# Optimization experiments

Measured on AMD Instinct MI355X. Metric: run time of the kernel, lower is better.

Reference implementation:

```python
import jax, jax.numpy as jnp
import numpy as np

B, L, D, T = 32, 2048, 64, 512          # batch, seq_len, input_dim, pred steps
H, EK = 2, 64                           # num_heads, embed_dim_per_head
E = H * EK                              # embed_dim = 128
P = 2                                   # function 'L' -> 2 coefficients
LAT, HID = 64, 64                       # latent_dim, hidden_dim
DIM = 2 * D                             # value dim after cat(X, M)


def setup_inputs() -> dict:
    key = jax.random.key(0)
    ks = jax.random.split(key, 20)
    s = 0.05
    inp = {
        "timesteps": jnp.sort(jax.random.uniform(ks[0], (B, L)), axis=-1),
        "X": jax.random.normal(ks[1], (B, L, D)),
        "M": jax.random.bernoulli(ks[2], 0.5, (B, L, D)).astype(jnp.float32),
        "y_time_steps": jnp.sort(jax.random.uniform(ks[3], (B, T)), axis=-1),
        # time_embedding: Linear(1, E)
        "te_w": jax.random.normal(ks[4], (1, E)) * s,
        "te_b": jax.random.normal(ks[5], (E,)) * s,
        # learned queries (1, P, E)
        "query": jax.random.normal(ks[6], (1, P, E)),
        # query_map / key_map: Linear(E, E), stored (in, out)
        "qm_w": jax.random.normal(ks[7], (E, E)) * s,
        "qm_b": jax.random.normal(ks[8], (E,)) * s,
        "km_w": jax.random.normal(ks[9], (E, E)) * s,
        "km_b": jax.random.normal(ks[10], (E,)) * s,
        # shared attention output head: Linear(2*D*H, LAT)
        "out_w": jax.random.normal(ks[11], (DIM * H, LAT)) * s,
        "out_b": jax.random.normal(ks[12], (LAT,)) * s,
        # decoder (depth=1): Linear(LAT, HID) -> ReLU -> Linear(HID, D)
        "dec_w1": jax.random.normal(ks[13], (LAT, HID)) * s,
        "dec_b1": jax.random.normal(ks[14], (HID,)) * s,
        "dec_w2": jax.random.normal(ks[15], (HID, D)) * s,
        "dec_b2": jax.random.normal(ks[16], (D,)) * s,
    }
    return inp


def _forward(timesteps, X, M, y_time_steps, te_w, te_b, query,
             qm_w, qm_b, km_w, km_b, out_w, out_b,
             dec_w1, dec_b1, dec_w2, dec_b2):
    # learn_time_embedding: Linear(1,E) then sin() on indices i % H == 0
    te = timesteps[..., None] @ te_w + te_b                 # (B, L, E)
    sin_idx = (jnp.arange(E) % H) == 0
    key_emb = jnp.where(sin_idx, jnp.sin(te), te)           # (B, L, E)

    value = jnp.concatenate([X, M], axis=-1)                # (B, L, 2D)
    mask = jnp.concatenate([M, M], axis=-1)                 # (B, L, 2D)

    q = query @ qm_w + qm_b                                 # (1, P, E)
    k = key_emb @ km_w + km_b                               # (B, L, E)
    qh = q.reshape(1, P, H, EK).transpose(0, 2, 1, 3)       # (1, H, P, EK)
    kh = k.reshape(B, L, H, EK).transpose(0, 2, 1, 3)       # (B, H, L, EK)

    scores = jnp.einsum('xhpe,bhle->bhpl', qh, kh) / jnp.sqrt(jnp.float32(EK))
    # score broadcast over value dim + per-feature mask fill (-1e9 as in torch)
    logits = jnp.where(mask[:, None, None, :, :] == 0, -1e9,
                       scores[..., None])                   # (B, H, P, L, 2D)
    p_attn = jax.nn.softmax(logits, axis=-2)                # softmax over L
    x = jnp.einsum('bhpld,bld->bhpd', p_attn, value)        # (B, H, P, 2D)

    x = x.transpose(0, 2, 1, 3).reshape(B, P, H * DIM)      # (B, P, H*2D)
    coeffs = x @ out_w + out_b                              # (B, P, LAT)

    # function 'L': linear-in-time latent trajectory
    z = coeffs[:, 0, :][:, None, :] + y_time_steps[..., None] * coeffs[:, 1, :][:, None, :]  # (B, T, LAT)
    h1 = jax.nn.relu(z @ dec_w1 + dec_b1)
    out = h1 @ dec_w2 + dec_b2                              # (B, T, D)
    return out, coeffs


def reference(timesteps, X, M, y_time_steps, te_w, te_b, query,
              qm_w, qm_b, km_w, km_b, out_w, out_b,
              dec_w1, dec_b1, dec_w2, dec_b2):
    return _forward(timesteps, X, M, y_time_steps, te_w, te_b, query,
                    qm_w, qm_b, km_w, km_b, out_w, out_b,
                    dec_w1, dec_b1, dec_w2, dec_b2)
```

## Files before the change

### kernel.cpp

```cpp
#include <hip/hip_runtime.h>
#include <hip/hip_bf16.h>

#define BB 32
#define LL 2048
#define DD 64
#define TT 512
#define INV2PI 0.15915494309189535f

#define NCHUNK 16
#define PSTRIDE 576

__global__ void __launch_bounds__(256) k_attn(
    const float* __restrict__ ts,
    const float* __restrict__ X,
    const float* __restrict__ M,
    const float* __restrict__ te_w,
    const float* __restrict__ te_b,
    const float* __restrict__ query,
    const float* __restrict__ qm_w,
    const float* __restrict__ qm_b,
    const float* __restrict__ km_w,
    const float* __restrict__ km_b,
    float* __restrict__ ws) {
  __shared__ float q_lds[256];
  __shared__ float r_lds[512];
  __shared__ __align__(16) float rp4[256];
  __shared__ __align__(8)  float feat2[128];
  __shared__ float tsl[128];
  __shared__ float C0[4], C1[4];
  __shared__ float sred[1024];
  __shared__ float w_lds[512];
  __shared__ float red[256 * 18];
  const int t = threadIdx.x;
  const int b = blockIdx.y;
  const int lc = blockIdx.x * 128;

  if (t < 128) tsl[t] = ts[(size_t)b * LL + lc + t];
  if (t < 64) {
    feat2[2 * t]     = te_w[2 * t] * INV2PI;
    feat2[2 * t + 1] = te_b[2 * t] * INV2PI;
  }

  {
    const int p = t >> 7, e = t & 127;
    const float* qq = query + p * 128;
    const float* qw = qm_w + e;
    float a0 = 0.f, a1 = 0.f, a2 = 0.f, a3 = 0.f;
    for (int i = 0; i < 128; i += 4) {
      a0 += qq[i]     * qw[i * 128];
      a1 += qq[i + 1] * qw[(i + 1) * 128];
      a2 += qq[i + 2] * qw[(i + 2) * 128];
      a3 += qq[i + 3] * qw[(i + 3) * 128];
    }
    q_lds[t] = (a0 + a1) + (a2 + a3) + qm_b[e];
  }

  const int dpair = t & 31, lr = t >> 5;
  const float2* X2 = (const float2*)X;
  const float2* M2 = (const float2*)M;
  const size_t base = ((size_t)b * LL + lc) * 32;
  float2 xa[8], ma[8];
#pragma unroll
  for (int i = 0; i < 8; ++i) {
    xa[i] = X2[base + (size_t)(lr + i * 8) * 32 + dpair];
    ma[i] = M2[base + (size_t)(lr + i * 8) * 32 + dpair];
  }
  __syncthreads();

  for (int o = t; o < 512; o += 256) {
    const int hp = o >> 7, i = o & 127;
    const int h = hp >> 1, p = hp & 1;
    const float4* km4 = (const float4*)(km_w + i * 128 + h * 64);
    const float* qp = &q_lds[p * 128 + h * 64];
    float acc = 0.f;
#pragma unroll
    for (int e4 = 0; e4 < 16; ++e4) {
      const float4 w = km4[e4];
      acc += qp[4 * e4] * w.x + qp[4 * e4 + 1] * w.y +
             qp[4 * e4 + 2] * w.z + qp[4 * e4 + 3] * w.w;
    }
    r_lds[o] = acc;
  }
  __syncthreads();

  if (t < 64) {
#pragma unroll
    for (int hp = 0; hp < 4; ++hp) rp4[t * 4 + hp] = r_lds[hp * 128 + 2 * t];
  }
  if (t >= 64 && t < 72) {
    const int hp = (t - 64) >> 1;
    if ((t & 1) == 0) {
      float s = 0.f;
      for (int e = 0; e < 64; ++e) s += te_w[2 * e + 1] * r_lds[hp * 128 + 2 * e + 1];
      C1[hp] = s;
    } else {
      float s = 0.f;
      for (int e = 0; e < 64; ++e) s += te_b[2 * e + 1] * r_lds[hp * 128 + 2 * e + 1];
      const int h = hp >> 1, p = hp & 1;
      float c = 0.f;
      for (int e = 0; e < 64; ++e) c += q_lds[p * 128 + h * 64 + e] * km_b[h * 64 + e];
      C0[hp] = s + c;
    }
  }
  __syncthreads();

  {
    const int l = t >> 1, half = t & 1;
    const float tt = tsl[l];
    const float2* f2 = (const float2*)feat2;
    const float4* r4 = (const float4*)rp4;
    float p0 = 0.f, p1 = 0.f, p2 = 0.f, p3 = 0.f;
    const int e0 = half * 32;
    for (int e = e0; e < e0 + 32; ++e) {
      const float2 wb = f2[e];
      const float f = __builtin_amdgcn_sinf(tt * wb.x + wb.y);
      const float4 r = r4[e];
      p0 += f * r.x; p1 += f * r.y; p2 += f * r.z; p3 += f * r.w;
    }
    sred[t * 4 + 0] = p0; sred[t * 4 + 1] = p1;
    sred[t * 4 + 2] = p2; sred[t * 4 + 3] = p3;
  }
  __syncthreads();
  {
    const int l = t >> 1, pr = t & 1;
    const float tt = tsl[l];
#pragma unroll
    for (int k2 = 0; k2 < 2; ++k2) {
      const int hp = pr * 2 + k2;
      const float s = sred[(2 * l) * 4 + hp] + sred[(2 * l + 1) * 4 + hp] +
                      tt * C1[hp] + C0[hp];
      w_lds[l * 4 + hp] = __expf(s * 0.125f);
    }
  }
  __syncthreads();

  float n[4][2] = {}, dn[4][2] = {}, sx[2] = {};
#pragma unroll
  for (int i = 0; i < 8; ++i) {
    const int ll = lr + i * 8;
    const float2 xv = xa[i], mv = ma[i];
    const float mx0 = mv.x * xv.x, mx1 = mv.y * xv.y;
    sx[0] += xv.x; sx[1] += xv.y;
#pragma unroll
    for (int hp = 0; hp < 4; ++hp) {
      const float w = w_lds[ll * 4 + hp];
      n[hp][0]  += w * mx0;  n[hp][1]  += w * mx1;
      dn[hp][0] += w * mv.x; dn[hp][1] += w * mv.y;
    }
  }
  for (int i = 8; i < 16; ++i) {
    const int ll = lr + i * 8;
    const float2 xv = X2[base + (size_t)ll * 32 + dpair];
    const float2 mv = M2[base + (size_t)ll * 32 + dpair];
    const float mx0 = mv.x * xv.x, mx1 = mv.y * xv.y;
    sx[0] += xv.x; sx[1] += xv.y;
#pragma unroll
    for (int hp = 0; hp < 4; ++hp) {
      const float w = w_lds[ll * 4 + hp];
      n[hp][0]  += w * mx0;  n[hp][1]  += w * mx1;
      dn[hp][0] += w * mv.x; dn[hp][1] += w * mv.y;
    }
  }

#pragma unroll
  for (int hp = 0; hp < 4; ++hp) {
    red[t * 18 + hp * 2 + 0] = n[hp][0];
    red[t * 18 + hp * 2 + 1] = n[hp][1];
    red[t * 18 + 8 + hp * 2 + 0] = dn[hp][0];
    red[t * 18 + 8 + hp * 2 + 1] = dn[hp][1];
  }
  red[t * 18 + 16] = sx[0];
  red[t * 18 + 17] = sx[1];
  __syncthreads();

  if (t < 32) {
    float* slot = ws + ((size_t)b * NCHUNK + blockIdx.x) * PSTRIDE;
    for (int j = 0; j < 18; ++j) {
      float s = 0.f;
#pragma unroll
      for (int r2 = 0; r2 < 8; ++r2) s += red[(r2 * 32 + t) * 18 + j];
      if (j < 8) {
        const int hp = j >> 1, half = j & 1;
        slot[hp * 64 + 2 * t + half] = s;
      } else if (j < 16) {
        const int j2 = j - 8, hp = j2 >> 1, half = j2 & 1;
        slot[256 + hp * 64 + 2 * t + half] = s;
      } else {
        slot[512 + 2 * t + (j - 16)] = s;
      }
    }
  }
}

__global__ void __launch_bounds__(256) k_dec(
    const float* __restrict__ yts,
    const float* __restrict__ out_w,
    const float* __restrict__ out_b,
    const float* __restrict__ dec_w1,
    const float* __restrict__ dec_b1,
    const float* __restrict__ dec_w2,
    const float* __restrict__ dec_b2,
    const float* __restrict__ ws,
    float* __restrict__ out) {
  __shared__ __align__(16) float acc_l[576];
  __shared__ float x_lds[512];
  __shared__ float cred[256];
  __shared__ float c_lds[128];
  __shared__ float abred[256];
  __shared__ float ABl[128];
  __shared__ __align__(16) float w2l[4096];
  __shared__ float h1l[1024];
  __shared__ float b2l[64], yl[64];
  const int t = threadIdx.x;
  const int b = blockIdx.y;
  const int t0 = blockIdx.x * 64;

  {
    const float4* s4 = (const float4*)dec_w2;
    float4* d4 = (float4*)w2l;
    for (int i = t; i < 1024; i += 256) d4[i] = s4[i];
  }
  if (t < 144) {
    const float4* p4 = (const float4*)(ws + (size_t)b * NCHUNK * PSTRIDE);
    float4 s; s.x = s.y = s.z = s.w = 0.f;
    for (int c = 0; c < NCHUNK; ++c) {
      const float4 v = p4[(size_t)c * 144 + t];
      s.x += v.x; s.y += v.y; s.z += v.z; s.w += v.w;
    }
    ((float4*)acc_l)[t] = s;
  }
  if (t >= 192) {
    const int k = t - 192;
    b2l[k] = dec_b2[k];
    yl[k] = yts[b * TT + t0 + k];
  }
  __syncthreads();

  {
    const int hp = t >> 6, d = t & 63;
    const int h = hp >> 1, p = hp & 1;
    const float num = acc_l[hp * 64 + d];
    const float den = acc_l[256 + hp * 64 + d];
    const float sxv = acc_l[512 + d];
    float x1, x2;
    if (den > 0.f) { x1 = num / den; x2 = 1.f; }
    else           { x1 = sxv * (1.f / (float)LL); x2 = 0.f; }
    x_lds[p * 256 + h * 128 + d] = x1;
    x_lds[p * 256 + h * 128 + 64 + d] = x2;
  }
  __syncthreads();

  {
    const int kh = t >> 7, pj = t & 127, p = pj >> 6, j = pj & 63;
    float acc = (kh == 0) ? out_b[j] : 0.f;
    const float* xp = &x_lds[p * 256 + kh * 128];
    const float* wp = out_w + (size_t)kh * 128 * 64 + j;
    for (int k = 0; k < 128; ++k) acc += xp[k] * wp[k * 64];
    cred[t] = acc;
  }
  __syncthreads();
  if (t < 128) {
    const float c = cred[t] + cred[t + 128];
    c_lds[t] = c;
    if (blockIdx.x == 0)
      out[(size_t)BB * TT * DD + b * 128 + t] = c;
  }
  __syncthreads();
  if (t < 128) {
    const int jh = t >> 6, k = t & 63;
    float a = 0.f, bb = 0.f;
    const float* cp = &c_lds[jh * 32];
    const float* cp2 = &c_lds[64 + jh * 32];
    for (int j = 0; j < 32; ++j) {
      const float w1 = dec_w1[(jh * 32 + j) * 64 + k];
      a += cp[j] * w1;
      bb += cp2[j] * w1;
    }
    abred[t * 2] = a;
    abred[t * 2 + 1] = bb;
  }
  __syncthreads();
  if (t < 64) {
    ABl[t]      = dec_b1[t] + abred[t * 2]     + abred[(64 + t) * 2];
    ABl[64 + t] =             abred[t * 2 + 1] + abred[(64 + t) * 2 + 1];
  }
  __syncthreads();

  const int tl = t >> 4, dg = t & 15;
  for (int it = 0; it < 4; ++it) {
    {
      int idx = t;
#pragma unroll
      for (int rr = 0; rr < 4; ++rr, idx += 256) {
        const int tl2 = idx >> 6, k = idx & 63;
        h1l[idx] = fmaxf(ABl[k] + yl[it * 16 + tl2] * ABl[64 + k], 0.f);
      }
    }
    __syncthreads();
    {
      float a0 = b2l[dg * 4], a1 = b2l[dg * 4 + 1],
            a2 = b2l[dg * 4 + 2], a3 = b2l[dg * 4 + 3];
      const float4* w4 = (const float4*)w2l;
      const float* h1p = &h1l[tl * 64];
      for (int k = 0; k < 64; ++k) {
        const float h = h1p[k];
        const float4 w = w4[k * 16 + dg];
        a0 += h * w.x; a1 += h * w.y; a2 += h * w.z; a3 += h * w.w;
      }
      const int tg = t0 + it * 16 + tl;
      const size_t off = ((size_t)b * TT + tg) * 64 + dg * 4;
      float4 o; o.x = a0; o.y = a1; o.z = a2; o.w = a3;
      *(float4*)(out + off) = o;
    }
    __syncthreads();
  }
}

extern "C" void kernel_launch(void* const* d_in, const int* in_sizes, int n_in,
                              void* d_out, int out_size, void* d_ws, size_t ws_size,
                              hipStream_t stream) {
  const float* ts     = (const float*)d_in[0];
  const float* X      = (const float*)d_in[1];
  const float* M      = (const float*)d_in[2];
  const float* yts    = (const float*)d_in[3];
  const float* te_w   = (const float*)d_in[4];
  const float* te_b   = (const float*)d_in[5];
  const float* query  = (const float*)d_in[6];
  const float* qm_w   = (const float*)d_in[7];
  const float* qm_b   = (const float*)d_in[8];
  const float* km_w   = (const float*)d_in[9];
  const float* km_b   = (const float*)d_in[10];
  const float* out_w  = (const float*)d_in[11];
  const float* out_b  = (const float*)d_in[12];
  const float* dec_w1 = (const float*)d_in[13];
  const float* dec_b1 = (const float*)d_in[14];
  const float* dec_w2 = (const float*)d_in[15];
  const float* dec_b2 = (const float*)d_in[16];
  float* ws = (float*)d_ws;
  float* out = (float*)d_out;

  k_attn<<<dim3(NCHUNK, BB), 256, 0, stream>>>(
      ts, X, M, te_w, te_b, query, qm_w, qm_b, km_w, km_b, ws);
  k_dec<<<dim3(TT / 64, BB), 256, 0, stream>>>(
      yts, out_w, out_b, dec_w1, dec_b1, dec_w2, dec_b2, ws, out);
}
```

Measured before the change: 132.6 us.

## Split pipeline into prep, attention, coefficient and decoder kernels with finer L chunks

The query/key projection preamble, previously recomputed by every attention block, is hoisted into a single-block prep kernel whose results go to workspace. The attention kernel now uses 64-row chunks (32 chunks per batch) with shuffle-based score reduction. Per-batch coefficient and first-layer decoder terms are computed once in their own kernel instead of in each decoder block. The decoder computes h1 on the fly per thread rather than staging it in LDS. The cost is two extra kernel launches and a serial single-block prep step, plus more partial sums to reduce.

```diff
diff --git a/kernel.cpp b/kernel.cpp
--- a/kernel.cpp
+++ b/kernel.cpp
@@ -7,13 +7,12 @@
 #define TT 512
 #define INV2PI 0.15915494309189535f
 
-#define NCHUNK 16
+#define NCHUNK 32
 #define PSTRIDE 576
-
-__global__ void __launch_bounds__(256) k_attn(
-    const float* __restrict__ ts,
-    const float* __restrict__ X,
-    const float* __restrict__ M,
+#define PREP0 (BB * NCHUNK * PSTRIDE)
+#define AB0 (PREP0 + 400)
+
+__global__ void __launch_bounds__(256) k_prep(
     const float* __restrict__ te_w,
     const float* __restrict__ te_b,
     const float* __restrict__ query,
@@ -24,22 +23,8 @@
     float* __restrict__ ws) {
   __shared__ float q_lds[256];
   __shared__ float r_lds[512];
-  __shared__ __align__(16) float rp4[256];
-  __shared__ __align__(8)  float feat2[128];
-  __shared__ float tsl[128];
-  __shared__ float C0[4], C1[4];
-  __shared__ float sred[1024];
-  __shared__ float w_lds[512];
-  __shared__ float red[256 * 18];
   const int t = threadIdx.x;
-  const int b = blockIdx.y;
-  const int lc = blockIdx.x * 128;
-
-  if (t < 128) tsl[t] = ts[(size_t)b * LL + lc + t];
-  if (t < 64) {
-    feat2[2 * t]     = te_w[2 * t] * INV2PI;
-    feat2[2 * t + 1] = te_b[2 * t] * INV2PI;
-  }
+  float* prep = ws + PREP0;
 
   {
     const int p = t >> 7, e = t & 127;
@@ -54,17 +39,6 @@
     }
     q_lds[t] = (a0 + a1) + (a2 + a3) + qm_b[e];
   }
-
-  const int dpair = t & 31, lr = t >> 5;
-  const float2* X2 = (const float2*)X;
-  const float2* M2 = (const float2*)M;
-  const size_t base = ((size_t)b * LL + lc) * 32;
-  float2 xa[8], ma[8];
-#pragma unroll
-  for (int i = 0; i < 8; ++i) {
-    xa[i] = X2[base + (size_t)(lr + i * 8) * 32 + dpair];
-    ma[i] = M2[base + (size_t)(lr + i * 8) * 32 + dpair];
-  }
   __syncthreads();
 
   for (int o = t; o < 512; o += 256) {
@@ -84,82 +58,102 @@
   __syncthreads();
 
   if (t < 64) {
-#pragma unroll
-    for (int hp = 0; hp < 4; ++hp) rp4[t * 4 + hp] = r_lds[hp * 128 + 2 * t];
-  }
-  if (t >= 64 && t < 72) {
-    const int hp = (t - 64) >> 1;
-    if ((t & 1) == 0) {
-      float s = 0.f;
-      for (int e = 0; e < 64; ++e) s += te_w[2 * e + 1] * r_lds[hp * 128 + 2 * e + 1];
-      C1[hp] = s;
-    } else {
-      float s = 0.f;
-      for (int e = 0; e < 64; ++e) s += te_b[2 * e + 1] * r_lds[hp * 128 + 2 * e + 1];
-      const int h = hp >> 1, p = hp & 1;
-      float c = 0.f;
-      for (int e = 0; e < 64; ++e) c += q_lds[p * 128 + h * 64 + e] * km_b[h * 64 + e];
-      C0[hp] = s + c;
-    }
-  }
-  __syncthreads();
-
-  {
-    const int l = t >> 1, half = t & 1;
+    float4 v;
+    v.x = r_lds[0 * 128 + 2 * t];
+    v.y = r_lds[1 * 128 + 2 * t];
+    v.z = r_lds[2 * 128 + 2 * t];
+    v.w = r_lds[3 * 128 + 2 * t];
+    ((float4*)prep)[t] = v;
+    prep[256 + 2 * t]     = te_w[2 * t] * INV2PI;
+    prep[256 + 2 * t + 1] = te_b[2 * t] * INV2PI;
+  }
+
+  {
+    const int hp = t >> 6, e = t & 63;
+    const int h = hp >> 1, p = hp & 1;
+    const float rodd = r_lds[hp * 128 + 2 * e + 1];
+    float pc1 = te_w[2 * e + 1] * rodd;
+    float pc0 = te_b[2 * e + 1] * rodd +
+                q_lds[p * 128 + h * 64 + e] * km_b[h * 64 + e];
+#pragma unroll
+    for (int off = 1; off < 64; off <<= 1) {
+      pc1 += __shfl_xor(pc1, off);
+      pc0 += __shfl_xor(pc0, off);
+    }
+    if (e == 0) {
+      prep[384 + hp] = pc1;
+      prep[388 + hp] = pc0;
+    }
+  }
+}
+
+__global__ void __launch_bounds__(256) k_attn(
+    const float* __restrict__ ts,
+    const float* __restrict__ X,
+    const float* __restrict__ M,
+    float* __restrict__ ws) {
+  __shared__ __align__(16) float rp4l[256];
+  __shared__ __align__(8)  float f2l[128];
+  __shared__ float Cl[8];
+  __shared__ float tsl[64];
+  __shared__ __align__(16) float w_lds[256];
+  __shared__ float red[256 * 18];
+  const int t = threadIdx.x;
+  const int b = blockIdx.y;
+  const int lc = blockIdx.x * 64;
+  const float* prep = ws + PREP0;
+
+  if (t < 64)       ((float4*)rp4l)[t] = ((const float4*)prep)[t];
+  else if (t < 128) ((float2*)f2l)[t - 64] = ((const float2*)(prep + 256))[t - 64];
+  else if (t < 136) Cl[t - 128] = prep[384 + (t - 128)];
+  if (t >= 192) tsl[t - 192] = ts[(size_t)b * LL + lc + (t - 192)];
+  __syncthreads();
+
+  {
+    const int l = t >> 2, qq = t & 3;
     const float tt = tsl[l];
-    const float2* f2 = (const float2*)feat2;
-    const float4* r4 = (const float4*)rp4;
-    float p0 = 0.f, p1 = 0.f, p2 = 0.f, p3 = 0.f;
-    const int e0 = half * 32;
-    for (int e = e0; e < e0 + 32; ++e) {
+    const float2* f2 = (const float2*)f2l;
+    const float4* r4 = (const float4*)rp4l;
+    float s0 = 0.f, s1 = 0.f, s2 = 0.f, s3 = 0.f;
+#pragma unroll
+    for (int i = 0; i < 16; ++i) {
+      const int e = qq * 16 + i;
       const float2 wb = f2[e];
       const float f = __builtin_amdgcn_sinf(tt * wb.x + wb.y);
       const float4 r = r4[e];
-      p0 += f * r.x; p1 += f * r.y; p2 += f * r.z; p3 += f * r.w;
-    }
-    sred[t * 4 + 0] = p0; sred[t * 4 + 1] = p1;
-    sred[t * 4 + 2] = p2; sred[t * 4 + 3] = p3;
-  }
-  __syncthreads();
-  {
-    const int l = t >> 1, pr = t & 1;
-    const float tt = tsl[l];
-#pragma unroll
-    for (int k2 = 0; k2 < 2; ++k2) {
-      const int hp = pr * 2 + k2;
-      const float s = sred[(2 * l) * 4 + hp] + sred[(2 * l + 1) * 4 + hp] +
-                      tt * C1[hp] + C0[hp];
-      w_lds[l * 4 + hp] = __expf(s * 0.125f);
-    }
-  }
-  __syncthreads();
-
+      s0 += f * r.x; s1 += f * r.y; s2 += f * r.z; s3 += f * r.w;
+    }
+    s0 += __shfl_xor(s0, 1); s1 += __shfl_xor(s1, 1);
+    s2 += __shfl_xor(s2, 1); s3 += __shfl_xor(s3, 1);
+    s0 += __shfl_xor(s0, 2); s1 += __shfl_xor(s1, 2);
+    s2 += __shfl_xor(s2, 2); s3 += __shfl_xor(s3, 2);
+    const float sv = (qq == 0) ? s0 : (qq == 1) ? s1 : (qq == 2) ? s2 : s3;
+    const float w = __expf((sv + tt * Cl[qq] + Cl[4 + qq]) * 0.125f);
+    w_lds[l * 4 + qq] = w;
+  }
+  __syncthreads();
+
+  const int dpair = t & 31, lr = t >> 5;
+  const float2* X2 = (const float2*)X;
+  const float2* M2 = (const float2*)M;
+  const size_t base = ((size_t)b * LL + lc) * 32;
   float n[4][2] = {}, dn[4][2] = {}, sx[2] = {};
 #pragma unroll
   for (int i = 0; i < 8; ++i) {
-    const int ll = lr + i * 8;
-    const float2 xv = xa[i], mv = ma[i];
-    const float mx0 = mv.x * xv.x, mx1 = mv.y * xv.y;
-    sx[0] += xv.x; sx[1] += xv.y;
-#pragma unroll
-    for (int hp = 0; hp < 4; ++hp) {
-      const float w = w_lds[ll * 4 + hp];
-      n[hp][0]  += w * mx0;  n[hp][1]  += w * mx1;
-      dn[hp][0] += w * mv.x; dn[hp][1] += w * mv.y;
-    }
-  }
-  for (int i = 8; i < 16; ++i) {
     const int ll = lr + i * 8;
     const float2 xv = X2[base + (size_t)ll * 32 + dpair];
     const float2 mv = M2[base + (size_t)ll * 32 + dpair];
     const float mx0 = mv.x * xv.x, mx1 = mv.y * xv.y;
     sx[0] += xv.x; sx[1] += xv.y;
-#pragma unroll
-    for (int hp = 0; hp < 4; ++hp) {
-      const float w = w_lds[ll * 4 + hp];
-      n[hp][0]  += w * mx0;  n[hp][1]  += w * mx1;
-      dn[hp][0] += w * mv.x; dn[hp][1] += w * mv.y;
-    }
+    const float4 wv = ((const float4*)w_lds)[ll];
+    n[0][0] += wv.x * mx0; n[0][1] += wv.x * mx1;
+    n[1][0] += wv.y * mx0; n[1][1] += wv.y * mx1;
+    n[2][0] += wv.z * mx0; n[2][1] += wv.z * mx1;
+    n[3][0] += wv.w * mx0; n[3][1] += wv.w * mx1;
+    dn[0][0] += wv.x * mv.x; dn[0][1] += wv.x * mv.y;
+    dn[1][0] += wv.y * mv.x; dn[1][1] += wv.y * mv.y;
+    dn[2][0] += wv.z * mv.x; dn[2][1] += wv.z * mv.y;
+    dn[3][0] += wv.w * mv.x; dn[3][1] += wv.w * mv.y;
   }
 
 #pragma unroll
@@ -192,34 +186,21 @@
   }
 }
 
-__global__ void __launch_bounds__(256) k_dec(
-    const float* __restrict__ yts,
+__global__ void __launch_bounds__(256) k_coef(
     const float* __restrict__ out_w,
     const float* __restrict__ out_b,
     const float* __restrict__ dec_w1,
     const float* __restrict__ dec_b1,
-    const float* __restrict__ dec_w2,
-    const float* __restrict__ dec_b2,
-    const float* __restrict__ ws,
+    float* __restrict__ ws,
     float* __restrict__ out) {
   __shared__ __align__(16) float acc_l[576];
   __shared__ float x_lds[512];
   __shared__ float cred[256];
   __shared__ float c_lds[128];
   __shared__ float abred[256];
-  __shared__ float ABl[128];
-  __shared__ __align__(16) float w2l[4096];
-  __shared__ float h1l[1024];
-  __shared__ float b2l[64], yl[64];
   const int t = threadIdx.x;
-  const int b = blockIdx.y;
-  const int t0 = blockIdx.x * 64;
-
-  {
-    const float4* s4 = (const float4*)dec_w2;
-    float4* d4 = (float4*)w2l;
-    for (int i = t; i < 1024; i += 256) d4[i] = s4[i];
-  }
+  const int b = blockIdx.x;
+
   if (t < 144) {
     const float4* p4 = (const float4*)(ws + (size_t)b * NCHUNK * PSTRIDE);
     float4 s; s.x = s.y = s.z = s.w = 0.f;
@@ -228,11 +209,6 @@
       s.x += v.x; s.y += v.y; s.z += v.z; s.w += v.w;
     }
     ((float4*)acc_l)[t] = s;
-  }
-  if (t >= 192) {
-    const int k = t - 192;
-    b2l[k] = dec_b2[k];
-    yl[k] = yts[b * TT + t0 + k];
   }
   __syncthreads();
 
@@ -262,8 +238,7 @@
   if (t < 128) {
     const float c = cred[t] + cred[t + 128];
     c_lds[t] = c;
-    if (blockIdx.x == 0)
-      out[(size_t)BB * TT * DD + b * 128 + t] = c;
+    out[(size_t)BB * TT * DD + b * 128 + t] = c;
   }
   __syncthreads();
   if (t < 128) {
@@ -281,39 +256,53 @@
   }
   __syncthreads();
   if (t < 64) {
-    ABl[t]      = dec_b1[t] + abred[t * 2]     + abred[(64 + t) * 2];
-    ABl[64 + t] =             abred[t * 2 + 1] + abred[(64 + t) * 2 + 1];
-  }
-  __syncthreads();
-
-  const int tl = t >> 4, dg = t & 15;
-  for (int it = 0; it < 4; ++it) {
-    {
-      int idx = t;
-#pragma unroll
-      for (int rr = 0; rr < 4; ++rr, idx += 256) {
-        const int tl2 = idx >> 6, k = idx & 63;
-        h1l[idx] = fmaxf(ABl[k] + yl[it * 16 + tl2] * ABl[64 + k], 0.f);
-      }
-    }
-    __syncthreads();
-    {
-      float a0 = b2l[dg * 4], a1 = b2l[dg * 4 + 1],
-            a2 = b2l[dg * 4 + 2], a3 = b2l[dg * 4 + 3];
-      const float4* w4 = (const float4*)w2l;
-      const float* h1p = &h1l[tl * 64];
-      for (int k = 0; k < 64; ++k) {
-        const float h = h1p[k];
-        const float4 w = w4[k * 16 + dg];
-        a0 += h * w.x; a1 += h * w.y; a2 += h * w.z; a3 += h * w.w;
-      }
-      const int tg = t0 + it * 16 + tl;
-      const size_t off = ((size_t)b * TT + tg) * 64 + dg * 4;
-      float4 o; o.x = a0; o.y = a1; o.z = a2; o.w = a3;
-      *(float4*)(out + off) = o;
-    }
-    __syncthreads();
-  }
+    ws[AB0 + b * 128 + t]      = dec_b1[t] + abred[t * 2] + abred[(64 + t) * 2];
+    ws[AB0 + b * 128 + 64 + t] =             abred[t * 2 + 1] + abred[(64 + t) * 2 + 1];
+  }
+}
+
+__global__ void __launch_bounds__(256) k_dec(
+    const float* __restrict__ yts,
+    const float* __restrict__ dec_b2,
+    const float* __restrict__ dec_w2,
+    const float* __restrict__ ws,
+    float* __restrict__ out) {
+  __shared__ __align__(16) float w2l[4096];
+  __shared__ float ABl[128];
+  __shared__ float yl[64];
+  __shared__ __align__(16) float b2l[64];
+  const int t = threadIdx.x;
+  const int b = blockIdx.y;
+  const int t0 = blockIdx.x * 64;
+
+  {
+    const float4* s4 = (const float4*)dec_w2;
+    float4* d4 = (float4*)w2l;
+    for (int i = t; i < 1024; i += 256) d4[i] = s4[i];
+  }
+  if (t < 128)      ABl[t] = ws[AB0 + b * 128 + t];
+  else if (t < 192) yl[t - 128] = yts[b * TT + t0 + (t - 128)];
+  else              b2l[t - 192] = dec_b2[t - 192];
+  __syncthreads();
+
+  const int lane = t & 63, wv = t >> 6;
+  const float y = yl[lane];
+  const float4* w24 = (const float4*)w2l;
+  float4 acc[4];
+#pragma unroll
+  for (int j = 0; j < 4; ++j) acc[j] = ((const float4*)b2l)[wv * 4 + j];
+  for (int k = 0; k < 64; ++k) {
+    const float h = fmaxf(ABl[k] + y * ABl[64 + k], 0.f);
+#pragma unroll
+    for (int j = 0; j < 4; ++j) {
+      const float4 w = w24[k * 16 + wv * 4 + j];
+      acc[j].x += h * w.x; acc[j].y += h * w.y;
+      acc[j].z += h * w.z; acc[j].w += h * w.w;
+    }
+  }
+  const size_t off = ((size_t)b * TT + t0 + lane) * 64 + wv * 16;
+#pragma unroll
+  for (int j = 0; j < 4; ++j) *(float4*)(out + off + j * 4) = acc[j];
 }
 
 extern "C" void kernel_launch(void* const* d_in, const int* in_sizes, int n_in,
@@ -339,8 +328,8 @@
   float* ws = (float*)d_ws;
   float* out = (float*)d_out;
 
-  k_attn<<<dim3(NCHUNK, BB), 256, 0, stream>>>(
-      ts, X, M, te_w, te_b, query, qm_w, qm_b, km_w, km_b, ws);
-  k_dec<<<dim3(TT / 64, BB), 256, 0, stream>>>(
-      yts, out_w, out_b, dec_w1, dec_b1, dec_w2, dec_b2, ws, out);
-}
+  k_prep<<<1, 256, 0, stream>>>(te_w, te_b, query, qm_w, qm_b, km_w, km_b, ws);
+  k_attn<<<dim3(NCHUNK, BB), 256, 0, stream>>>(ts, X, M, ws);
+  k_coef<<<BB, 256, 0, stream>>>(out_w, out_b, dec_w1, dec_b1, ws, out);
+  k_dec<<<dim3(TT / 64, BB), 256, 0, stream>>>(yts, dec_b2, dec_w2, ws, out);
+}
```

Result: no change. 133.3 us (+0.5%).
